# Performance work log

Hardware: AMD Instinct MI355X
Metric: run time of the kernel (lower is better)

The kernel has to match this reference:

```python
import jax, jax.numpy as jnp
import numpy as np

HIDDEN = 2048
NUM_ROUTED = 24          # num_routed_experts(6) * segmentation_factor(4)
ROUTED_INTER = 512       # intermediate_dim(2048) // segmentation_factor(4)
NUM_SHARED = 2
SHARED_INTER = 2048
TOP_K = 6


def setup_inputs() -> dict:
    key = jax.random.key(0)
    ks = jax.random.split(key, 8)
    std = 0.02
    x = jax.random.normal(ks[0], (2, 2048, HIDDEN), dtype=jnp.float32)
    gate_w = jax.random.normal(ks[1], (NUM_ROUTED, HIDDEN), dtype=jnp.float32) * (0.02 / np.sqrt(HIDDEN))
    shared_w1 = jax.random.normal(ks[2], (NUM_SHARED, HIDDEN, SHARED_INTER), dtype=jnp.float32) * std
    shared_w3 = jax.random.normal(ks[3], (NUM_SHARED, HIDDEN, SHARED_INTER), dtype=jnp.float32) * std
    shared_w2 = jax.random.normal(ks[4], (NUM_SHARED, SHARED_INTER, HIDDEN), dtype=jnp.float32) * std
    routed_w1 = jax.random.normal(ks[5], (NUM_ROUTED, HIDDEN, ROUTED_INTER), dtype=jnp.float32) * std
    routed_w3 = jax.random.normal(ks[6], (NUM_ROUTED, HIDDEN, ROUTED_INTER), dtype=jnp.float32) * std
    routed_w2 = jax.random.normal(ks[7], (NUM_ROUTED, ROUTED_INTER, HIDDEN), dtype=jnp.float32) * std
    return {"x": x, "gate_w": gate_w,
            "shared_w1": shared_w1, "shared_w2": shared_w2, "shared_w3": shared_w3,
            "routed_w1": routed_w1, "routed_w2": routed_w2, "routed_w3": routed_w3}


def _swiglu_ffn(x, w1, w2, w3):
    # x: [..., n, h]; w1,w3: [..., h, i]; w2: [..., i, h]  (dropout inactive at eval)
    h = jax.nn.silu(jnp.einsum('nh,ehi->eni', x, w1)) * jnp.einsum('nh,ehi->eni', x, w3)
    return jnp.einsum('eni,eih->enh', h, w2)


def reference(x, gate_w, shared_w1, shared_w2, shared_w3, routed_w1, routed_w2, routed_w3):
    B, S, H = x.shape
    x_flat = x.reshape(-1, H)                       # [N, H]
    N = x_flat.shape[0]

    # shared experts (summed)
    shared_out = _swiglu_ffn(x_flat, shared_w1, shared_w2, shared_w3).sum(axis=0)  # [N, H]

    # routing (eval mode: no bias added to logits, aux_loss = 0)
    scores = jax.nn.sigmoid(x_flat @ gate_w.T)      # [N, E]
    top_scores, top_idx = jax.lax.top_k(scores, TOP_K)
    top_weights = top_scores / (top_scores.sum(-1, keepdims=True) + 1e-9)  # [N, K]

    # dense dispatch/combine weights [N, E] (indices unique per row)
    dense_w = jnp.zeros((N, NUM_ROUTED), dtype=x.dtype)
    dense_w = dense_w.at[jnp.arange(N)[:, None], top_idx].set(top_weights)

    # run every routed expert on all tokens, combine with routing weights
    expert_out = _swiglu_ffn(x_flat, routed_w1, routed_w2, routed_w3)  # [E, N, H]
    combined = jnp.einsum('ne,enh->nh', dense_w, expert_out)

    output = (shared_out + combined).reshape(B, S, H)
    aux_loss = jnp.float32(0.0)  # eval mode
    return output, aux_loss
```

## Files before the change

### kernel.cpp

```cpp
#include <hip/hip_runtime.h>
#include <hip/hip_bf16.h>

#define HID   2048
#define NTOK  4096
#define NEXP  24
#define SHCOL 4096
#define TOPK  6
#define NSLOT (NTOK * TOPK)

typedef __bf16 bf16_t;
typedef __bf16 bf16x8 __attribute__((ext_vector_type(8)));
typedef __bf16 bf16x4 __attribute__((ext_vector_type(4)));
typedef float  f32x4  __attribute__((ext_vector_type(4)));

__device__ __forceinline__ void async_copy16(const bf16_t* g, bf16_t* l) {
  __builtin_amdgcn_global_load_lds(
      (const __attribute__((address_space(1))) unsigned int*)g,
      (__attribute__((address_space(3))) unsigned int*)l,
      16, 0, 0);
}
template<int N> __device__ __forceinline__ void wait_vm() {
  asm volatile("s_waitcnt vmcnt(%0)" :: "n"(N) : "memory");
}
__device__ __forceinline__ void memfence_sched() { asm volatile("" ::: "memory"); }

__device__ __forceinline__ bf16x8 frag32(const bf16_t* region, int row, int cc) {
  return *(const bf16x8*)(region + row * 32 + ((cc ^ ((row >> 1) & 3)) << 3));
}

__global__ void cast_x_kernel(const float* __restrict__ x, bf16_t* __restrict__ xb) {
  int i = blockIdx.x * 256 + threadIdx.x;
  float4 v = ((const float4*)x)[i];
  bf16x4 o = { (bf16_t)v.x, (bf16_t)v.y, (bf16_t)v.z, (bf16_t)v.w };
  ((bf16x4*)xb)[i] = o;
}

__global__ __launch_bounds__(256) void transpose_cast_v2(
    const float* __restrict__ src, bf16_t* __restrict__ dst,
    int C, long dstStride, long srcExpStride, long dstExpStride) {
  __shared__ float t[64][68];
  const int e = blockIdx.z;
  src += (long)e * srcExpStride;
  dst += (long)e * dstExpStride;
  const int c0 = blockIdx.x * 64, r0 = blockIdx.y * 64;
  const int tid = threadIdx.x;
  {
    const int tr = tid >> 4, tc = tid & 15;
#pragma unroll
    for (int p = 0; p < 4; ++p) {
      const int r = p * 16 + tr;
      const float4 v = *(const float4*)(src + (long)(r0 + r) * C + c0 + tc * 4);
      *(float4*)&t[r][tc * 4] = v;
    }
  }
  __syncthreads();
  {
    const int l8 = tid & 7, rb = l8 * 8;
#pragma unroll
    for (int p = 0; p < 2; ++p) {
      const int c = p * 32 + (tid >> 3);
      bf16x8 o;
#pragma unroll
      for (int s = 0; s < 8; ++s) o[s] = (bf16_t)t[rb + s][c];
      *(bf16x8*)(dst + (long)(c0 + c) * dstStride + r0 + rb) = o;
    }
  }
}

__global__ void gate_topk(const float* __restrict__ x, const float* __restrict__ gw,
                          int* __restrict__ tk_idx, float* __restrict__ tk_w,
                          float* __restrict__ aux) {
  int lane = threadIdx.x & 63;
  int wave = threadIdx.x >> 6;
  int token = blockIdx.x * 4 + wave;
  const float* xr = x + (long)token * HID;
  float xv[32];
#pragma unroll
  for (int i = 0; i < 32; ++i) xv[i] = xr[lane + i * 64];
  float sc[NEXP];
#pragma unroll
  for (int e = 0; e < NEXP; ++e) {
    const float* g = gw + (long)e * HID;
    float s = 0.f;
#pragma unroll
    for (int i = 0; i < 32; ++i) s += xv[i] * g[lane + i * 64];
#pragma unroll
    for (int off = 32; off > 0; off >>= 1) s += __shfl_down(s, off);
    sc[e] = s;
  }
  if (lane == 0) {
    float sg[NEXP];
#pragma unroll
    for (int e = 0; e < NEXP; ++e) sg[e] = 1.0f / (1.0f + expf(-sc[e]));
    unsigned taken = 0;
    int   sel[TOPK];
    float sw[TOPK];
    float sum = 0.f;
    for (int k = 0; k < TOPK; ++k) {
      float best = -1.f; int bi = 0;
#pragma unroll
      for (int e = 0; e < NEXP; ++e) {
        bool avail = !(taken & (1u << e));
        if (avail && sg[e] > best) { best = sg[e]; bi = e; }
      }
      taken |= (1u << bi);
      sel[k] = bi; sw[k] = best; sum += best;
    }
    float inv = 1.0f / (sum + 1e-9f);
#pragma unroll
    for (int k = 0; k < TOPK; ++k) {
      tk_idx[token * TOPK + k] = sel[k];
      tk_w[token * TOPK + k]   = sw[k] * inv;
    }
  }
  if (blockIdx.x == 0 && threadIdx.x == 0) *aux = 0.0f;
}

__global__ void dispatch(const int* __restrict__ tk_idx, const float* __restrict__ tk_w,
                         int* __restrict__ perm, float* __restrict__ wslot,
                         int* __restrict__ slot_of, int* __restrict__ meta,
                         int* __restrict__ uptab, int* __restrict__ dntab) {
  __shared__ int cnt[NEXP], cnt2[NEXP], off[NEXP + 1];
  int tid = threadIdx.x;
  if (tid < NEXP) { cnt[tid] = 0; cnt2[tid] = 0; }
  __syncthreads();
  for (int i = tid; i < NSLOT; i += 1024) atomicAdd(&cnt[tk_idx[i]], 1);
  __syncthreads();
  if (tid == 0) {
    int o = 0, un = 0, dn = 0;
    for (int e = 0; e < NEXP; ++e) {
      off[e] = o;
      int c = cnt[e];
      for (int r0 = 0; r0 < c; r0 += 256) uptab[un++] = (e << 16) | r0;
      for (int r0 = 0; r0 < c; r0 += 128) dntab[dn++] = (e << 16) | r0;
      o += c;
    }
    off[NEXP] = o;
    meta[0] = un; meta[1] = dn;
    for (int e = 0; e < NEXP; ++e) { meta[8 + e] = cnt[e]; meta[32 + e] = off[e]; }
  }
  __syncthreads();
  for (int i = tid; i < NSLOT; i += 1024) {
    int e = tk_idx[i];
    int loc = atomicAdd(&cnt2[e], 1);
    int slot = off[e] + loc;
    perm[slot] = i / TOPK;
    wslot[slot] = tk_w[i];
    slot_of[i] = slot;
  }
}

__global__ __launch_bounds__(512, 2) void gemm_up(
    const bf16_t* __restrict__ xb, const bf16_t* __restrict__ w1t,
    const bf16_t* __restrict__ w3t, bf16_t* __restrict__ hsh,
    bf16_t* __restrict__ hr, const int* __restrict__ perm,
    const float* __restrict__ wslot, const int* __restrict__ meta,
    const int* __restrict__ uptab) {
  __shared__ bf16_t lds[4 * 16384];
  const int bid = blockIdx.x;
  const int tid  = threadIdx.x;
  const int lane = tid & 63;
  const int wave = tid >> 6;
  const int wm = wave >> 2;
  const int wc = wave & 3;
  const bool role_sh = bid < 512;
  int m0 = 0, j0 = 0, jc = 0, M = 256, bslot = 0;
  const bf16_t *b1G, *b3G;
  if (role_sh) {
    m0 = (bid >> 5) * 256; j0 = (bid & 31) * 128;
    b1G = w1t + (long)j0 * HID;
    b3G = w3t + (long)j0 * HID;
  } else {
    int t = bid - 512;
    int rt = t >> 2; jc = t & 3;
    if (rt >= meta[0]) return;
    int pk = uptab[rt];
    int e = pk >> 16, row0 = pk & 0xffff;
    bslot = meta[32 + e] + row0;
    M = min(256, meta[8 + e] - row0);
    int col = SHCOL + e * 512 + jc * 128;
    b1G = w1t + (long)col * HID;
    b3G = w3t + (long)col * HID;
  }
  const bf16_t* gsrc[4];
  int loff[4];
#pragma unroll
  for (int it = 0; it < 4; ++it) {
    int idx = it * 512 + tid;
    if (idx < 1024) {
      int r = idx >> 2, c = idx & 3;
      long rowbase;
      if (role_sh) rowbase = (long)(m0 + r) * HID;
      else         rowbase = (long)perm[bslot + ((r < M) ? r : 0)] * HID;
      gsrc[it] = xb + rowbase + ((c ^ ((r >> 1) & 3)) << 3);
      loff[it] = idx << 3;
    } else if (idx < 1536) {
      int i2 = idx - 1024; int r = i2 >> 2, c = i2 & 3;
      gsrc[it] = b1G + (long)r * HID + ((c ^ ((r >> 1) & 3)) << 3);
      loff[it] = 8192 + (i2 << 3);
    } else {
      int i2 = idx - 1536; int r = i2 >> 2, c = i2 & 3;
      gsrc[it] = b3G + (long)r * HID + ((c ^ ((r >> 1) & 3)) << 3);
      loff[it] = 12288 + (i2 << 3);
    }
  }
  auto STAGE = [&](int t) {
    bf16_t* sb = lds + (t & 3) * 16384;
#pragma unroll
    for (int it = 0; it < 4; ++it)
      async_copy16(gsrc[it] + t * 32, sb + loff[it]);
  };

  f32x4 acc1[8][2] = {};
  f32x4 acc3[8][2] = {};
  const int NT = HID / 32;
  STAGE(0); STAGE(1);
  for (int t = 0; t < NT; ++t) {
    if (t + 2 < NT) STAGE(t + 2);
    if (t < NT - 2)       wait_vm<8>();
    else if (t == NT - 2) wait_vm<4>();
    else                  wait_vm<0>();
    __builtin_amdgcn_s_barrier();
    memfence_sched();
    const bf16_t* sb = lds + (t & 3) * 16384;
    const int rA = wm * 128 + (lane & 15);
    const int cc = lane >> 4;
    bf16x8 a[8];
#pragma unroll
    for (int fm = 0; fm < 8; ++fm) a[fm] = frag32(sb, rA + fm * 16, cc);
    __builtin_amdgcn_s_setprio(1);
#pragma unroll
    for (int fn = 0; fn < 2; ++fn) {
      const int rB = wc * 32 + fn * 16 + (lane & 15);
      bf16x8 b1 = frag32(sb + 8192,  rB, cc);
      bf16x8 b3 = frag32(sb + 12288, rB, cc);
#pragma unroll
      for (int fm = 0; fm < 8; ++fm) {
        acc1[fm][fn] = __builtin_amdgcn_mfma_f32_16x16x32_bf16(a[fm], b1, acc1[fm][fn], 0, 0, 0);
        acc3[fm][fn] = __builtin_amdgcn_mfma_f32_16x16x32_bf16(a[fm], b3, acc3[fm][fn], 0, 0, 0);
      }
    }
    __builtin_amdgcn_s_setprio(0);
    memfence_sched();
  }
  const int mloc_base = wm * 128 + ((lane >> 4) << 2);
  const int cloc = wc * 32 + (lane & 15);
#pragma unroll
  for (int fm = 0; fm < 8; ++fm) {
#pragma unroll
    for (int jj = 0; jj < 4; ++jj) {
      const int mloc = mloc_base + fm * 16 + jj;
      if (role_sh) {
        bf16_t* dst = hsh + (long)(m0 + mloc) * SHCOL + j0 + cloc;
#pragma unroll
        for (int fn = 0; fn < 2; ++fn) {
          const float u1 = acc1[fm][fn][jj];
          const float u3 = acc3[fm][fn][jj];
          dst[fn * 16] = (bf16_t)((u1 / (1.0f + __expf(-u1))) * u3);
        }
      } else if (mloc < M) {
        const int slot = bslot + mloc;
        const float w = wslot[slot];
        bf16_t* dst = hr + (long)slot * 512 + jc * 128 + cloc;
#pragma unroll
        for (int fn = 0; fn < 2; ++fn) {
          const float u1 = acc1[fm][fn][jj];
          const float u3 = acc3[fm][fn][jj];
          dst[fn * 16] = (bf16_t)((u1 / (1.0f + __expf(-u1))) * u3 * w);
        }
      }
    }
  }
}

__global__ __launch_bounds__(512, 2) void gemm_down(
    const bf16_t* __restrict__ hsh, const bf16_t* __restrict__ w2ts,
    const bf16_t* __restrict__ hr, const bf16_t* __restrict__ rw2t,
    float* __restrict__ sout, bf16_t* __restrict__ y,
    const int* __restrict__ meta, const int* __restrict__ dntab) {
  __shared__ bf16_t lds[4 * 12288];
  const int bid = blockIdx.x;
  const int tid  = threadIdx.x;
  const int lane = tid & 63;
  const int wave = tid >> 6;
  const int wm = wave >> 2;
  const int wc = wave & 3;
  const bool role_sh = bid < 256;
  int m0 = 0, n0, M = 128, bslot = 0, NT;
  const bf16_t *aG, *bG;
  long lda, ldb;
  if (role_sh) {
    m0 = (bid >> 3) * 128; n0 = (bid & 7) * 256;
    aG = hsh + (long)m0 * SHCOL; lda = SHCOL;
    bG = w2ts + (long)n0 * SHCOL; ldb = SHCOL;
    NT = SHCOL / 32;
  } else {
    int t = bid - 256;
    int rt = t >> 3; n0 = (t & 7) * 256;
    if (rt >= meta[1]) return;
    int pk = dntab[rt];
    int e = pk >> 16, row0 = pk & 0xffff;
    bslot = meta[32 + e] + row0;
    M = min(128, meta[8 + e] - row0);
    aG = hr + (long)bslot * 512; lda = 512;
    bG = rw2t + (long)e * (2048L * 512) + (long)n0 * 512; ldb = 512;
    NT = 512 / 32;
  }
  const bf16_t* gsrc[3];
  int loff[3];
#pragma unroll
  for (int it = 0; it < 3; ++it) {
    int idx = it * 512 + tid;
    if (idx < 512) {
      int r = idx >> 2, c = idx & 3;
      gsrc[it] = aG + (long)r * lda + ((c ^ ((r >> 1) & 3)) << 3);
      loff[it] = idx << 3;
    } else {
      int i2 = idx - 512; int r = i2 >> 2, c = i2 & 3;
      gsrc[it] = bG + (long)r * ldb + ((c ^ ((r >> 1) & 3)) << 3);
      loff[it] = 4096 + (i2 << 3);
    }
  }
  auto STAGE = [&](int t) {
    bf16_t* sb = lds + (t & 3) * 12288;
#pragma unroll
    for (int it = 0; it < 3; ++it)
      async_copy16(gsrc[it] + t * 32, sb + loff[it]);
  };

  f32x4 acc[4][4] = {};
  STAGE(0); STAGE(1);
  for (int t = 0; t < NT; ++t) {
    if (t + 2 < NT) STAGE(t + 2);
    if (t < NT - 2)       wait_vm<6>();
    else if (t == NT - 2) wait_vm<3>();
    else                  wait_vm<0>();
    __builtin_amdgcn_s_barrier();
    memfence_sched();
    const bf16_t* sb = lds + (t & 3) * 12288;
    const int rA = wm * 64 + (lane & 15);
    const int cc = lane >> 4;
    bf16x8 a[4];
#pragma unroll
    for (int fm = 0; fm < 4; ++fm) a[fm] = frag32(sb, rA + fm * 16, cc);
    __builtin_amdgcn_s_setprio(1);
#pragma unroll
    for (int fn = 0; fn < 4; ++fn) {
      bf16x8 b = frag32(sb + 4096, wc * 64 + fn * 16 + (lane & 15), cc);
#pragma unroll
      for (int fm = 0; fm < 4; ++fm)
        acc[fm][fn] = __builtin_amdgcn_mfma_f32_16x16x32_bf16(a[fm], b, acc[fm][fn], 0, 0, 0);
    }
    __builtin_amdgcn_s_setprio(0);
    memfence_sched();
  }
  const int mloc_base = wm * 64 + ((lane >> 4) << 2);
  const int cbase = n0 + wc * 64 + (lane & 15);
#pragma unroll
  for (int fm = 0; fm < 4; ++fm)
#pragma unroll
    for (int jj = 0; jj < 4; ++jj) {
      const int mloc = mloc_base + fm * 16 + jj;
      if (role_sh) {
#pragma unroll
        for (int fn = 0; fn < 4; ++fn)
          sout[(long)(m0 + mloc) * HID + cbase + fn * 16] = acc[fm][fn][jj];
      } else if (mloc < M) {
#pragma unroll
        for (int fn = 0; fn < 4; ++fn)
          y[(long)(bslot + mloc) * HID + cbase + fn * 16] = (bf16_t)acc[fm][fn][jj];
      }
    }
}

__global__ void combine(const float* __restrict__ sout, const bf16_t* __restrict__ y,
                        const int* __restrict__ slot_of, float* __restrict__ out) {
  const int n = blockIdx.x;
  const int c0 = threadIdx.x * 8;
  float acc[8];
  const float4* sp = (const float4*)(sout + (long)n * HID + c0);
  float4 s0 = sp[0], s1 = sp[1];
  acc[0]=s0.x; acc[1]=s0.y; acc[2]=s0.z; acc[3]=s0.w;
  acc[4]=s1.x; acc[5]=s1.y; acc[6]=s1.z; acc[7]=s1.w;
#pragma unroll
  for (int k = 0; k < TOPK; ++k) {
    int slot = slot_of[n * TOPK + k];
    bf16x8 v = *(const bf16x8*)(y + (long)slot * HID + c0);
#pragma unroll
    for (int i = 0; i < 8; ++i) acc[i] += (float)v[i];
  }
  float4* op = (float4*)(out + (long)n * HID + c0);
  op[0] = make_float4(acc[0], acc[1], acc[2], acc[3]);
  op[1] = make_float4(acc[4], acc[5], acc[6], acc[7]);
}

__global__ void fill_sentinel(float* out, int n) {
  for (int i = blockIdx.x * 256 + threadIdx.x; i < n; i += gridDim.x * 256)
    out[i] = 12345.0f;
}

extern "C" void kernel_launch(void* const* d_in, const int* in_sizes, int n_in,
                              void* d_out, int out_size, void* d_ws, size_t ws_size,
                              hipStream_t stream) {
  (void)in_sizes; (void)n_in;
  const float* x   = (const float*)d_in[0];
  const float* gw  = (const float*)d_in[1];
  const float* sw1 = (const float*)d_in[2];
  const float* sw2 = (const float*)d_in[3];
  const float* sw3 = (const float*)d_in[4];
  const float* rw1 = (const float*)d_in[5];
  const float* rw2 = (const float*)d_in[6];
  const float* rw3 = (const float*)d_in[7];
  float* out = (float*)d_out;

  const size_t OFF_XB    = 0;
  const size_t OFF_W1T   = 16777216;
  const size_t OFF_W3T   = 83886080;
  const size_t OFF_W2TS  = 150994944;
  const size_t OFF_RW2T  = 167772160;
  const size_t OFF_HSH   = 218103808;
  const size_t OFF_HR    = 251658240;
  const size_t OFF_SOUT  = 277086208;
  const size_t OFF_TKI   = 310640640;
  const size_t OFF_TKW   = 310738944;
  const size_t OFF_PERM  = 310837248;
  const size_t OFF_WSLOT = 310935552;
  const size_t OFF_SLOTOF= 311033856;
  const size_t OFF_META  = 311132160;
  const size_t OFF_UPTAB = 311136256;
  const size_t OFF_DNTAB = 311140352;
  const size_t NEED      = 311148544;
  if (ws_size < NEED) {
    fill_sentinel<<<4096, 256, 0, stream>>>(out, out_size);
    return;
  }
  char* ws = (char*)d_ws;
  bf16_t* xb     = (bf16_t*)(ws + OFF_XB);
  bf16_t* w1t    = (bf16_t*)(ws + OFF_W1T);
  bf16_t* w3t    = (bf16_t*)(ws + OFF_W3T);
  bf16_t* w2ts   = (bf16_t*)(ws + OFF_W2TS);
  bf16_t* rw2t   = (bf16_t*)(ws + OFF_RW2T);
  bf16_t* hsh    = (bf16_t*)(ws + OFF_HSH);
  bf16_t* hr     = (bf16_t*)(ws + OFF_HR);
  float*  sout   = (float*)(ws + OFF_SOUT);
  bf16_t* y      = (bf16_t*)(ws + OFF_W1T);
  int*    tki    = (int*)(ws + OFF_TKI);
  float*  tkw    = (float*)(ws + OFF_TKW);
  int*    perm   = (int*)(ws + OFF_PERM);
  float*  wslot  = (float*)(ws + OFF_WSLOT);
  int*    slotof = (int*)(ws + OFF_SLOTOF);
  int*    meta   = (int*)(ws + OFF_META);
  int*    uptab  = (int*)(ws + OFF_UPTAB);
  int*    dntab  = (int*)(ws + OFF_DNTAB);

  cast_x_kernel<<<8192, 256, 0, stream>>>(x, xb);
  gate_topk<<<1024, 256, 0, stream>>>(x, gw, tki, tkw, out + (size_t)NTOK * HID);
  dispatch<<<1, 1024, 0, stream>>>(tki, tkw, perm, wslot, slotof, meta, uptab, dntab);

  transpose_cast_v2<<<dim3(32, 32, 2),  256, 0, stream>>>(sw1, w1t, 2048, 2048, 2048L*2048, 2048L*2048);
  transpose_cast_v2<<<dim3(8,  32, 24), 256, 0, stream>>>(rw1, w1t + (long)SHCOL*HID, 512, 2048, 2048L*512, 512L*2048);
  transpose_cast_v2<<<dim3(32, 32, 2),  256, 0, stream>>>(sw3, w3t, 2048, 2048, 2048L*2048, 2048L*2048);
  transpose_cast_v2<<<dim3(8,  32, 24), 256, 0, stream>>>(rw3, w3t + (long)SHCOL*HID, 512, 2048, 2048L*512, 512L*2048);
  transpose_cast_v2<<<dim3(32, 32, 2),  256, 0, stream>>>(sw2, w2ts, 2048, 4096, 2048L*2048, 2048);
  transpose_cast_v2<<<dim3(32, 8, 24),  256, 0, stream>>>(rw2, rw2t, 2048, 512, 512L*2048, 2048L*512);

  gemm_up<<<dim3(512 + 480), 512, 0, stream>>>(xb, w1t, w3t, hsh, hr, perm, wslot, meta, uptab);
  gemm_down<<<dim3(256 + 1728), 512, 0, stream>>>(hsh, w2ts, hr, rw2t, sout, y, meta, dntab);
  combine<<<dim3(NTOK), 256, 0, stream>>>(sout, y, slotof, out);
}
```

Baseline: 666.4 us.

## Split GEMM main loops into two phases with interleaved LDS reads and barriers

Both the gate/up GEMM and the down GEMM main loops are restructured into a two-phase schedule. The first half of the fragments is read from LDS before the next async stage is issued, then half the MFMAs run, the remaining fragments are loaded between extra barriers, and the second half of the MFMAs follows. The vmcnt wait moves to the end of each iteration. The goal is to overlap LDS reads with MFMA work across waves and to cut peak fragment register pressure. In exchange it adds several barriers per K-step, and it relies on the 4-deep ring buffer to avoid hazards when the wait is moved.

```diff
diff --git a/kernel.cpp b/kernel.cpp
--- a/kernel.cpp
+++ b/kernel.cpp
@@ -23,6 +23,11 @@
   asm volatile("s_waitcnt vmcnt(%0)" :: "n"(N) : "memory");
 }
 __device__ __forceinline__ void memfence_sched() { asm volatile("" ::: "memory"); }
+__device__ __forceinline__ void bar() {
+  memfence_sched();
+  __builtin_amdgcn_s_barrier();
+  memfence_sched();
+}
 
 __device__ __forceinline__ bf16x8 frag32(const bf16_t* region, int row, int cc) {
   return *(const bf16x8*)(region + row * 32 + ((cc ^ ((row >> 1) & 3)) << 3));
@@ -215,33 +220,50 @@
   f32x4 acc3[8][2] = {};
   const int NT = HID / 32;
   STAGE(0); STAGE(1);
+  wait_vm<4>();
+  __syncthreads();
+  const int rA = wm * 128 + (lane & 15);
+  const int rB = wc * 32 + (lane & 15);
+  const int cc = lane >> 4;
   for (int t = 0; t < NT; ++t) {
+    const bf16_t* sb = lds + (t & 3) * 16384;
+    bf16x8 a[4], b1[2], b3[2];
+#pragma unroll
+    for (int fm = 0; fm < 4; ++fm) a[fm] = frag32(sb, rA + fm * 16, cc);
+#pragma unroll
+    for (int fn = 0; fn < 2; ++fn) {
+      b1[fn] = frag32(sb + 8192,  rB + fn * 16, cc);
+      b3[fn] = frag32(sb + 12288, rB + fn * 16, cc);
+    }
     if (t + 2 < NT) STAGE(t + 2);
-    if (t < NT - 2)       wait_vm<8>();
-    else if (t == NT - 2) wait_vm<4>();
-    else                  wait_vm<0>();
-    __builtin_amdgcn_s_barrier();
-    memfence_sched();
-    const bf16_t* sb = lds + (t & 3) * 16384;
-    const int rA = wm * 128 + (lane & 15);
-    const int cc = lane >> 4;
-    bf16x8 a[8];
-#pragma unroll
-    for (int fm = 0; fm < 8; ++fm) a[fm] = frag32(sb, rA + fm * 16, cc);
+    bar();
     __builtin_amdgcn_s_setprio(1);
 #pragma unroll
-    for (int fn = 0; fn < 2; ++fn) {
-      const int rB = wc * 32 + fn * 16 + (lane & 15);
-      bf16x8 b1 = frag32(sb + 8192,  rB, cc);
-      bf16x8 b3 = frag32(sb + 12288, rB, cc);
-#pragma unroll
-      for (int fm = 0; fm < 8; ++fm) {
-        acc1[fm][fn] = __builtin_amdgcn_mfma_f32_16x16x32_bf16(a[fm], b1, acc1[fm][fn], 0, 0, 0);
-        acc3[fm][fn] = __builtin_amdgcn_mfma_f32_16x16x32_bf16(a[fm], b3, acc3[fm][fn], 0, 0, 0);
+    for (int fn = 0; fn < 2; ++fn)
+#pragma unroll
+      for (int fm = 0; fm < 4; ++fm) {
+        acc1[fm][fn] = __builtin_amdgcn_mfma_f32_16x16x32_bf16(a[fm], b1[fn], acc1[fm][fn], 0, 0, 0);
+        acc3[fm][fn] = __builtin_amdgcn_mfma_f32_16x16x32_bf16(a[fm], b3[fn], acc3[fm][fn], 0, 0, 0);
       }
-    }
+    __builtin_amdgcn_s_setprio(0);
+    bar();
+    bf16x8 a2[4];
+#pragma unroll
+    for (int fm = 0; fm < 4; ++fm) a2[fm] = frag32(sb, rA + 64 + fm * 16, cc);
+    bar();
+    __builtin_amdgcn_s_setprio(1);
+#pragma unroll
+    for (int fn = 0; fn < 2; ++fn)
+#pragma unroll
+      for (int fm = 0; fm < 4; ++fm) {
+        acc1[4 + fm][fn] = __builtin_amdgcn_mfma_f32_16x16x32_bf16(a2[fm], b1[fn], acc1[4 + fm][fn], 0, 0, 0);
+        acc3[4 + fm][fn] = __builtin_amdgcn_mfma_f32_16x16x32_bf16(a2[fm], b3[fn], acc3[4 + fm][fn], 0, 0, 0);
+      }
     __builtin_amdgcn_s_setprio(0);
     memfence_sched();
+    if (t < NT - 2) wait_vm<4>();
+    else            wait_vm<0>();
+    bar();
   }
   const int mloc_base = wm * 128 + ((lane >> 4) << 2);
   const int cloc = wc * 32 + (lane & 15);
@@ -330,29 +352,42 @@
 
   f32x4 acc[4][4] = {};
   STAGE(0); STAGE(1);
+  wait_vm<3>();
+  __syncthreads();
+  const int rA = wm * 64 + (lane & 15);
+  const int rB = wc * 64 + (lane & 15);
+  const int cc = lane >> 4;
   for (int t = 0; t < NT; ++t) {
+    const bf16_t* sb = lds + (t & 3) * 12288;
+    bf16x8 a[4], b[4];
+#pragma unroll
+    for (int fm = 0; fm < 4; ++fm) a[fm] = frag32(sb, rA + fm * 16, cc);
+    b[0] = frag32(sb + 4096, rB, cc);
+    b[1] = frag32(sb + 4096, rB + 16, cc);
     if (t + 2 < NT) STAGE(t + 2);
-    if (t < NT - 2)       wait_vm<6>();
-    else if (t == NT - 2) wait_vm<3>();
-    else                  wait_vm<0>();
-    __builtin_amdgcn_s_barrier();
-    memfence_sched();
-    const bf16_t* sb = lds + (t & 3) * 12288;
-    const int rA = wm * 64 + (lane & 15);
-    const int cc = lane >> 4;
-    bf16x8 a[4];
-#pragma unroll
-    for (int fm = 0; fm < 4; ++fm) a[fm] = frag32(sb, rA + fm * 16, cc);
+    bar();
     __builtin_amdgcn_s_setprio(1);
 #pragma unroll
-    for (int fn = 0; fn < 4; ++fn) {
-      bf16x8 b = frag32(sb + 4096, wc * 64 + fn * 16 + (lane & 15), cc);
+    for (int fn = 0; fn < 2; ++fn)
 #pragma unroll
       for (int fm = 0; fm < 4; ++fm)
-        acc[fm][fn] = __builtin_amdgcn_mfma_f32_16x16x32_bf16(a[fm], b, acc[fm][fn], 0, 0, 0);
-    }
+        acc[fm][fn] = __builtin_amdgcn_mfma_f32_16x16x32_bf16(a[fm], b[fn], acc[fm][fn], 0, 0, 0);
+    __builtin_amdgcn_s_setprio(0);
+    bar();
+    b[2] = frag32(sb + 4096, rB + 32, cc);
+    b[3] = frag32(sb + 4096, rB + 48, cc);
+    bar();
+    __builtin_amdgcn_s_setprio(1);
+#pragma unroll
+    for (int fn = 2; fn < 4; ++fn)
+#pragma unroll
+      for (int fm = 0; fm < 4; ++fm)
+        acc[fm][fn] = __builtin_amdgcn_mfma_f32_16x16x32_bf16(a[fm], b[fn], acc[fm][fn], 0, 0, 0);
     __builtin_amdgcn_s_setprio(0);
     memfence_sched();
+    if (t < NT - 2) wait_vm<3>();
+    else            wait_vm<0>();
+    bar();
   }
   const int mloc_base = wm * 64 + ((lane >> 4) << 2);
   const int cbase = n0 + wc * 64 + (lane & 15);
```

New measurement: 682.4 us. 1.02x slower.
